# Kernel tuning notes

Hardware: AMD Instinct MI355X
Metric: run time of the kernel (lower is better)

## Reference

```python
import jax, jax.numpy as jnp
import numpy as np

EPS = 1e-5

def _ln(x, g, b):
    m = jnp.mean(x, axis=-1, keepdims=True)
    v = jnp.mean((x - m) ** 2, axis=-1, keepdims=True)
    return (x - m) * jax.lax.rsqrt(v + EPS) * g + b

def setup_inputs() -> dict:
    key = jax.random.key(0)
    B, T, V, D = 32, 512, 16, 128
    ks = jax.random.split(key, 22)
    rn = lambda k, shp, sc: jax.random.normal(k, shp, jnp.float32) * sc
    inp = {
        "x": rn(ks[0], (B, T, V), 1.0),
        # per-variable GRN params (stacked over the V variables)
        "W1": rn(ks[1], (V, D), 1.0),          # fc1: Linear(1, D) weight per var
        "b1": rn(ks[2], (V, D), 0.02),
        "W2": rn(ks[3], (V, D, D), 1.0 / np.sqrt(D)),   # fc2: Linear(D, D)
        "b2": rn(ks[4], (V, D), 0.02),
        "Wg": rn(ks[5], (V, D, D), 1.0 / np.sqrt(D)),   # gate: Linear(D, D)
        "bg": rn(ks[6], (V, D), 0.02),
        "Ws": rn(ks[7], (V, D), 1.0),          # skip: Linear(1, D)
        "bs": rn(ks[8], (V, D), 0.02),
        "gamma": jnp.ones((V, D), jnp.float32),
        "beta": jnp.zeros((V, D), jnp.float32),
        # softmax GRN params: d_in = V*D, d_hidden = D, d_out = V
        "sW1": rn(ks[9], (D, V * D), 1.0 / np.sqrt(V * D)),
        "sb1": rn(ks[10], (D,), 0.02),
        "sW2": rn(ks[11], (V, D), 1.0 / np.sqrt(D)),
        "sb2": rn(ks[12], (V,), 0.02),
        "sWg": rn(ks[13], (V, D), 1.0 / np.sqrt(D)),
        "sbg": rn(ks[14], (V,), 0.02),
        "sWs": rn(ks[15], (V, V * D), 1.0 / np.sqrt(V * D)),
        "sbs": rn(ks[16], (V,), 0.02),
        "sgamma": jnp.ones((V,), jnp.float32),
        "sbeta": jnp.zeros((V,), jnp.float32),
    }
    return inp

def reference(x, W1, b1, W2, b2, Wg, bg, Ws, bs, gamma, beta,
              sW1, sb1, sW2, sb2, sWg, sbg, sWs, sbs, sgamma, sbeta):
    V, D = W1.shape
    lead = x.shape[:-1]
    xf = x.reshape(-1, V)                                  # (N, V)
    # ---- all per-variable GRNs batched over the var dim ----
    h = jax.nn.elu(xf[..., None] * W1 + b1)                # (N, V, D)
    h2 = jnp.einsum('nvd,vod->nvo', h, W2) + b2            # (N, V, D)
    g = jax.nn.sigmoid(jnp.einsum('nvd,vod->nvo', h, Wg) + bg)
    skip = xf[..., None] * Ws + bs                         # (N, V, D)
    stacked = _ln(g * h2 + (1.0 - g) * skip, gamma, beta)  # (N, V, D)
    # ---- softmax GRN over flattened embeddings ----
    flat = stacked.reshape(-1, V * D)                      # (N, V*D)
    hs = jax.nn.elu(flat @ sW1.T + sb1)                    # (N, D)
    h2s = hs @ sW2.T + sb2                                 # (N, V)
    gs = jax.nn.sigmoid(hs @ sWg.T + sbg)
    sks = flat @ sWs.T + sbs
    weights = jax.nn.softmax(_ln(gs * h2s + (1.0 - gs) * sks, sgamma, sbeta), axis=-1)
    processed = jnp.einsum('nvd,nv->nd', stacked, weights) # (N, D)
    return processed.reshape(*lead, D), weights.reshape(*lead, V)
```

## Files before the change

### kernel.cpp

```cpp
#include <hip/hip_runtime.h>
#include <hip/hip_bf16.h>
#include <math.h>

#define NVAR 16
#define ND 128
#define NVD 2048
#define NROWS 16384
#define RTA 256
#define NRB 32

typedef short s16x8 __attribute__((ext_vector_type(8)));
typedef short s16x4 __attribute__((ext_vector_type(4)));
typedef float f32x4 __attribute__((ext_vector_type(4)));
typedef unsigned short u16;

#define MFMA(a,b,c) __builtin_amdgcn_mfma_f32_16x16x32_bf16((a),(b),(c),0,0,0)

#define OFF_W2  0
#define OFF_WG  262144
#define OFF_SW1 524288
#define OFF_SWS 786432
#define OFF_SW2 819200
#define OFF_SWG 821248
#define WS_ELEMS 823296
#define OFF_STK 823296
#define STK_ELEMS ((size_t)NROWS*NVD)
#define WS_NEEDED_BYTES (((size_t)WS_ELEMS + STK_ELEMS)*2)
#define SV_ELEMS ((size_t)(NROWS/16)*2048)

__device__ __forceinline__ unsigned f2bf(float f){
    union { float f; unsigned u; } c; c.f = f;
    unsigned u = c.u;
    u += 0x7fffu + ((u >> 16) & 1u);
    return u >> 16;
}
__device__ __forceinline__ float bf2f(unsigned bits){
    union { unsigned u; float f; } c; c.u = bits << 16;
    return c.f;
}
__device__ __forceinline__ float eluf(float x){ return x > 0.f ? x : __expf(x) - 1.f; }
__device__ __forceinline__ float sigm(float x){
    return __builtin_amdgcn_rcpf(1.f + __expf(-x));
}

__device__ __forceinline__ int offHs(int r, int c){
    return r*128 + ((((c>>3) ^ (r&7))<<3) | (c&7));
}
__device__ __forceinline__ int offBig(int r, int c){
    return r*2048 + ((((c>>3) ^ (r&7))<<3) | (c&7));
}

__global__ void prep_kernel(const float* __restrict__ W2, const float* __restrict__ Wg,
                            const float* __restrict__ sW1, const float* __restrict__ sWs,
                            const float* __restrict__ sW2, const float* __restrict__ sWg,
                            u16* __restrict__ ws){
    int i = blockIdx.x*256 + threadIdx.x;
    if (i >= WS_ELEMS) return;
    float v;
    if      (i < OFF_WG)  v = W2[i];
    else if (i < OFF_SW1) v = Wg[i-OFF_WG];
    else if (i < OFF_SWS) v = sW1[i-OFF_SW1];
    else if (i < OFF_SW2) v = sWs[i-OFF_SWS];
    else if (i < OFF_SWG) v = sW2[i-OFF_SW2];
    else                  v = sWg[i-OFF_SWG];
    ws[i] = (u16)f2bf(v);
}

__global__ __launch_bounds__(512, 2)
void vsn_varA(const float* __restrict__ x,
              const float* __restrict__ W1, const float* __restrict__ b1,
              const float* __restrict__ b2, const float* __restrict__ bg,
              const float* __restrict__ Wsk, const float* __restrict__ bsk,
              const float* __restrict__ gamma, const float* __restrict__ beta,
              u16* __restrict__ ws)
{
    __shared__ u16 lw2[128*128];
    __shared__ u16 lwg[128*128];
    __shared__ float lp[8*128];
    __shared__ float lxv[RTA];

    const int t = threadIdx.x, w = t>>6, l = t&63;
    const int hr = l>>4, c16 = l&15;
    const int v = blockIdx.y;
    const int row0 = blockIdx.x*RTA;

    #pragma unroll
    for (int i=0;i<8;++i){
        int cid = i*512 + t;
        int mat = cid>>11, within = cid&2047;
        int r = within>>4, c8 = within&15;
        const u16* src = ws + (mat? OFF_WG:OFF_W2) + v*16384 + r*128 + c8*8;
        s16x8 val = *reinterpret_cast<const s16x8*>(src);
        u16* dst = (mat? lwg:lw2) + r*128 + ((c8 ^ (r&7))<<3);
        *reinterpret_cast<s16x8*>(dst) = val;
    }
    if (t < 128){
        lp[t]     = W1[v*ND+t];    lp[128+t] = b1[v*ND+t];
        lp[256+t] = b2[v*ND+t];    lp[384+t] = bg[v*ND+t];
        lp[512+t] = Wsk[v*ND+t];   lp[640+t] = bsk[v*ND+t];
        lp[768+t] = gamma[v*ND+t]; lp[896+t] = beta[v*ND+t];
    }
    if (t < RTA) lxv[t] = x[(size_t)(row0+t)*NVAR + v];
    __syncthreads();

    #pragma unroll 1
    for (int pass=0; pass<2; ++pass){
        const int lrow0 = (w + pass*8)*16;
        const float xv = lxv[lrow0 + c16];

        s16x8 B[4];
        #pragma unroll
        for (int ks=0;ks<4;++ks){
            s16x8 o;
            #pragma unroll
            for (int j=0;j<8;++j){
                int c = ks*32 + hr*8 + j;
                o[j] = (short)f2bf(eluf(xv*lp[c] + lp[128+c]));
            }
            B[ks] = o;
        }
        __builtin_amdgcn_sched_barrier(0);

        float y[8][4];
        #pragma unroll
        for (int ct=0; ct<8; ++ct){
            f32x4 a2 = {0.f,0.f,0.f,0.f}, ag = {0.f,0.f,0.f,0.f};
            const int wr = ct*16 + c16;
            #pragma unroll
            for (int ks=0;ks<4;++ks){
                int chunk = (ks*4 + hr) ^ (wr&7);
                s16x8 A2 = *reinterpret_cast<const s16x8*>(lw2 + wr*128 + chunk*8);
                a2 = MFMA(A2, B[ks], a2);
            }
            #pragma unroll
            for (int ks=0;ks<4;++ks){
                int chunk = (ks*4 + hr) ^ (wr&7);
                s16x8 Ag = *reinterpret_cast<const s16x8*>(lwg + wr*128 + chunk*8);
                ag = MFMA(Ag, B[ks], ag);
            }
            const int obb = ct*16 + hr*4;
            float4 b2v = *reinterpret_cast<const float4*>(&lp[256+obb]);
            float4 bgv = *reinterpret_cast<const float4*>(&lp[384+obb]);
            float4 wsv = *reinterpret_cast<const float4*>(&lp[512+obb]);
            float4 bsv = *reinterpret_cast<const float4*>(&lp[640+obb]);
            #pragma unroll
            for (int j=0;j<4;++j){
                float h2 = a2[j] + reinterpret_cast<const float*>(&b2v)[j];
                float gg = sigm(ag[j] + reinterpret_cast<const float*>(&bgv)[j]);
                float sk = xv*reinterpret_cast<const float*>(&wsv)[j]
                           + reinterpret_cast<const float*>(&bsv)[j];
                y[ct][j] = gg*h2 + (1.f-gg)*sk;
            }
            __builtin_amdgcn_sched_barrier(0);
        }
        float s = 0.f, q = 0.f;
        #pragma unroll
        for (int ct=0;ct<8;++ct)
            #pragma unroll
            for (int j=0;j<4;++j){ float yy = y[ct][j]; s += yy; q += yy*yy; }
        s += __shfl_xor(s, 16); s += __shfl_xor(s, 32);
        q += __shfl_xor(q, 16); q += __shfl_xor(q, 32);
        float mean = s*(1.f/ND);
        float inv  = rsqrtf(q*(1.f/ND) - mean*mean + 1e-5f);

        const int grp = blockIdx.x*16 + w + pass*8;
        u16* stkb = ws + OFF_STK + (size_t)v*SV_ELEMS + (size_t)grp*2048;
        #pragma unroll
        for (int ctp=0; ctp<4; ++ctp){
            s16x4 o0, o1;
            {
                int ct = ctp*2;
                const int obb = ct*16 + hr*4;
                float4 gm = *reinterpret_cast<const float4*>(&lp[768+obb]);
                float4 bt = *reinterpret_cast<const float4*>(&lp[896+obb]);
                #pragma unroll
                for (int j=0;j<4;++j){
                    float z = (y[ct][j]-mean)*inv*reinterpret_cast<const float*>(&gm)[j]
                              + reinterpret_cast<const float*>(&bt)[j];
                    o0[j] = (short)f2bf(z);
                }
            }
            {
                int ct = ctp*2 + 1;
                const int obb = ct*16 + hr*4;
                float4 gm = *reinterpret_cast<const float4*>(&lp[768+obb]);
                float4 bt = *reinterpret_cast<const float4*>(&lp[896+obb]);
                #pragma unroll
                for (int j=0;j<4;++j){
                    float z = (y[ct][j]-mean)*inv*reinterpret_cast<const float*>(&gm)[j]
                              + reinterpret_cast<const float*>(&bt)[j];
                    o1[j] = (short)f2bf(z);
                }
            }
            u16* bp = stkb + ctp*512 + c16*32;
            *reinterpret_cast<s16x4*>(bp + hr*4)      = o0;
            *reinterpret_cast<s16x4*>(bp + 16 + hr*4) = o1;
            __builtin_amdgcn_sched_barrier(0);
        }
    }
}

__device__ __forceinline__ s16x8 ldA(const u16* abuf, int vrel, int rg, int ctp, int n, int hr){
    int base = (((vrel*2 + rg)*4 + ctp)*16 + n)*32;
    int fn = (n>>1)&3;
    return *reinterpret_cast<const s16x8*>(abuf + base + ((hr ^ fn)<<3));
}

__global__ __launch_bounds__(512, 4)
void vsn_softB(const u16* __restrict__ ws,
               const float* __restrict__ sb1, const float* __restrict__ sb2,
               const float* __restrict__ sbg, const float* __restrict__ sbs,
               const float* __restrict__ sgamma, const float* __restrict__ sbeta,
               float* __restrict__ out_proc, float* __restrict__ out_w)
{
    __shared__ u16   abuf[8192];
    __shared__ u16   hsb[32*128];
    __shared__ float pps_[4*32*16];
    __shared__ float pph[32*16];
    __shared__ float ppg[32*16];
    __shared__ float sksf[32*16];
    __shared__ float wgtb[32*16];

    float* pps = pps_;

    const int t = threadIdx.x, w = t>>6, l = t&63;
    const int hr = l>>4, c16 = l&15;
    const int row0 = blockIdx.x * NRB;
    const int grp0 = row0 >> 4;
    const int orow = w*16 + c16;
    const int rgs = w & 1;
    const int khf = w >> 1;

    const u16* stk  = ws + OFF_STK;
    const u16* sW1b = ws + OFF_SW1;
    const u16* sWsb = ws + OFF_SWS;

    f32x4 accHs[2] = {{0,0,0,0},{0,0,0,0}};
    f32x4 accSk = {0,0,0,0};

    #pragma unroll 1
    for (int kt=0; kt<8; ++kt){
        #pragma unroll
        for (int i=0;i<2;++i){
            int cid = i*512 + t;
            int vv  = kt*2 + (cid>>9);
            int rg  = (cid>>8)&1;
            int n   = (cid>>2)&15;
            int u   = cid&3;
            const u16* src = stk + (size_t)vv*SV_ELEMS + (size_t)(grp0+rg)*2048
                           + ((cid>>2)&63)*32 + u*8;
            s16x8 val = *reinterpret_cast<const s16x8*>(src);
            *reinterpret_cast<s16x8*>(abuf + (cid>>2)*32 + ((u ^ ((n>>1)&3))<<3)) = val;
        }
        __syncthreads();
        #pragma unroll
        for (int ks=0; ks<8; ++ks){
            s16x8 bf = *reinterpret_cast<const s16x8*>(
                sW1b + (size_t)orow*NVD + kt*256 + ks*32 + hr*8);
            #pragma unroll
            for (int rg=0; rg<2; ++rg){
                s16x8 af = ldA(abuf, ks>>2, rg, ks&3, c16, hr);
                accHs[rg] = MFMA(af, bf, accHs[rg]);
            }
        }
        #pragma unroll
        for (int kk=0; kk<2; ++kk){
            int ks = khf*2 + kk;
            s16x8 bf = *reinterpret_cast<const s16x8*>(
                sWsb + (size_t)c16*NVD + kt*256 + ks*32 + hr*8);
            s16x8 af = ldA(abuf, ks>>2, rgs, ks&3, c16, hr);
            accSk = MFMA(af, bf, accSk);
        }
        __syncthreads();
    }

    {
        float bb = sb1[orow];
        #pragma unroll
        for (int rg=0; rg<2; ++rg){
            #pragma unroll
            for (int j=0;j<4;++j){
                int r = rg*16 + hr*4 + j;
                hsb[offHs(r, orow)] = (u16)f2bf(eluf(accHs[rg][j] + bb));
            }
        }
        #pragma unroll
        for (int j=0;j<4;++j)
            pps[khf*512 + (rgs*16 + hr*4 + j)*16 + c16] = accSk[j];
    }
    __syncthreads();

    sksf[t] = pps[t] + pps[512+t] + pps[1024+t] + pps[1536+t] + sbs[t&15];
    if (w < 4){
        const u16* Bsrc = (w < 2) ? (ws + OFF_SW2) : (ws + OFF_SWG);
        int rg = w & 1;
        f32x4 acc = {0,0,0,0};
        #pragma unroll
        for (int ks=0; ks<4; ++ks){
            int rr = rg*16 + c16;
            int chunk = (ks*4 + hr) ^ (rr&7);
            s16x8 af = *reinterpret_cast<const s16x8*>(hsb + rr*128 + chunk*8);
            s16x8 bf = *reinterpret_cast<const s16x8*>(Bsrc + c16*ND + ks*32 + hr*8);
            acc = MFMA(af, bf, acc);
        }
        float* dst = (w < 2) ? pph : ppg;
        #pragma unroll
        for (int j=0;j<4;++j)
            dst[(rg*16 + hr*4 + j)*16 + c16] = acc[j];
    }
    __syncthreads();

    {
        int r = t>>4, vv = t & 15;
        float h2s = pph[r*16+vv] + sb2[vv];
        float gs  = sigm(ppg[r*16+vv] + sbg[vv]);
        float yv  = gs*h2s + (1.f-gs)*sksf[r*16+vv];
        float ssum = yv, qsum = yv*yv;
        #pragma unroll
        for (int m=1;m<16;m<<=1){ ssum += __shfl_xor(ssum,m,16); qsum += __shfl_xor(qsum,m,16); }
        float mean = ssum*(1.f/NVAR);
        float var  = qsum*(1.f/NVAR) - mean*mean;
        float z = (yv-mean)*rsqrtf(var+1e-5f)*sgamma[vv] + sbeta[vv];
        float mx = z;
        #pragma unroll
        for (int m=1;m<16;m<<=1) mx = fmaxf(mx, __shfl_xor(mx,m,16));
        float e = __expf(z-mx);
        float es = e;
        #pragma unroll
        for (int m=1;m<16;m<<=1) es += __shfl_xor(es,m,16);
        float wgt = e * __builtin_amdgcn_rcpf(es);
        wgtb[r*16+vv] = wgt;
        out_w[(size_t)(row0+r)*NVAR + vv] = wgt;
    }
    __syncthreads();

    {
        int r = t>>4, cu = t&15;
        int ctp = cu>>2, u = cu&3;
        int grp = (row0+r)>>4, n = r&15;
        float acc[8] = {0,0,0,0,0,0,0,0};
        #pragma unroll
        for (int v=0; v<NVAR; ++v){
            float wv = wgtb[r*16 + v];
            const u16* sp = stk + (size_t)v*SV_ELEMS + (size_t)grp*2048
                          + (ctp*16+n)*32 + u*8;
            s16x8 sv = *reinterpret_cast<const s16x8*>(sp);
            #pragma unroll
            for (int k=0;k<8;++k) acc[k] += bf2f((u16)sv[k]) * wv;
        }
        float* op = out_proc + (size_t)(row0+r)*ND + ctp*32 + u*8;
        float4 lo = { acc[0], acc[1], acc[2], acc[3] };
        float4 hi = { acc[4], acc[5], acc[6], acc[7] };
        *reinterpret_cast<float4*>(op)     = lo;
        *reinterpret_cast<float4*>(op + 4) = hi;
    }
}

__global__ __launch_bounds__(512, 4)
void vsn_fused(const float* __restrict__ x,
               const float* __restrict__ W1, const float* __restrict__ b1,
               const float* __restrict__ b2, const float* __restrict__ bg,
               const float* __restrict__ Wsk, const float* __restrict__ bsk,
               const float* __restrict__ gamma, const float* __restrict__ beta,
               const float* __restrict__ sb1, const float* __restrict__ sb2,
               const float* __restrict__ sbg, const float* __restrict__ sbs,
               const float* __restrict__ sgamma, const float* __restrict__ sbeta,
               const u16* __restrict__ ws,
               float* __restrict__ out_proc, float* __restrict__ out_w)
{
    __shared__ u16   big[16*2048];
    __shared__ u16   hsb[16*128];
    __shared__ float pp[8*256];
    __shared__ float psumbuf[256];
    __shared__ float sksbuf[256];
    __shared__ float sx[256];

    float* psum  = psumbuf;
    float* psum2 = psumbuf + 128;

    const int t   = threadIdx.x;
    const int w   = t >> 6;
    const int l   = t & 63;
    const int hr  = l >> 4;
    const int c16 = l & 15;
    const int row0 = blockIdx.x * 16;
    const int orow = w*16 + c16;

    if (t < 256) sx[t] = x[row0*NVAR + t];
    __syncthreads();

    const u16* W2b = ws + OFF_W2;
    const u16* Wgb = ws + OFF_WG;

    for (int v = 0; v < NVAR; ++v){
        #pragma unroll
        for (int i = 0; i < 4; ++i){
            int idx = i*512 + t;
            int r = idx >> 7, d = idx & 127;
            float hv = eluf(sx[r*NVAR+v]*W1[v*ND+d] + b1[v*ND+d]);
            big[offBig(r, v*ND+d)] = (u16)f2bf(hv);
        }
        __syncthreads();

        s16x8 A[4];
        #pragma unroll
        for (int ks = 0; ks < 4; ++ks)
            A[ks] = *reinterpret_cast<const s16x8*>(&big[offBig(c16, v*ND + ks*32 + hr*8)]);
        const s16x8* B2p = reinterpret_cast<const s16x8*>(W2b + v*ND*ND + orow*ND + hr*8);
        const s16x8* Bgp = reinterpret_cast<const s16x8*>(Wgb + v*ND*ND + orow*ND + hr*8);
        f32x4 acc2 = {0.f,0.f,0.f,0.f}, accg = {0.f,0.f,0.f,0.f};
        #pragma unroll
        for (int ks = 0; ks < 4; ++ks) acc2 = MFMA(A[ks], B2p[ks*4], acc2);
        #pragma unroll
        for (int ks = 0; ks < 4; ++ks) accg = MFMA(A[ks], Bgp[ks*4], accg);

        const float b2v = b2[v*ND+orow], bgv = bg[v*ND+orow];
        const float wsv = Wsk[v*ND+orow], bsv = bsk[v*ND+orow];
        float y[4];
        #pragma unroll
        for (int j = 0; j < 4; ++j){
            int r = hr*4 + j;
            float h2 = acc2[j] + b2v;
            float g  = sigm(accg[j] + bgv);
            float sk = sx[r*NVAR+v]*wsv + bsv;
            y[j] = g*h2 + (1.f-g)*sk;
        }
        float s[4], q[4];
        #pragma unroll
        for (int j=0;j<4;++j){ s[j]=y[j]; q[j]=y[j]*y[j]; }
        #pragma unroll
        for (int m=1; m<16; m<<=1){
            #pragma unroll
            for (int j=0;j<4;++j){
                s[j] += __shfl_xor(s[j], m, 16);
                q[j] += __shfl_xor(q[j], m, 16);
            }
        }
        if (c16 == 0){
            #pragma unroll
            for (int j=0;j<4;++j){
                psum [(hr*4+j)*8 + w] = s[j];
                psum2[(hr*4+j)*8 + w] = q[j];
            }
        }
        __syncthreads();

        if (t < 16){
            float ss=0.f, qq=0.f;
            #pragma unroll
            for (int ww=0; ww<8; ++ww){ ss += psum[t*8+ww]; qq += psum2[t*8+ww]; }
            float mean = ss*(1.f/ND);
            float var  = qq*(1.f/ND) - mean*mean;
            sksbuf[t]      = mean;
            sksbuf[16 + t] = rsqrtf(var + 1e-5f);
        }
        __syncthreads();

        const float gm = gamma[v*ND+orow], bt = beta[v*ND+orow];
        #pragma unroll
        for (int j=0;j<4;++j){
            int r = hr*4 + j;
            float z = (y[j]-sksbuf[r])*sksbuf[16+r]*gm + bt;
            big[offBig(r, v*ND+orow)] = (u16)f2bf(z);
        }
    }
    __syncthreads();

    const u16* sW1b = ws + OFF_SW1;
    {
        f32x4 acc0 = {0,0,0,0}, acc1 = {0,0,0,0};
        const s16x8* Bp = reinterpret_cast<const s16x8*>(sW1b + orow*NVD + hr*8);
        #pragma unroll 8
        for (int ks = 0; ks < 64; ks += 2){
            s16x8 A0 = *reinterpret_cast<const s16x8*>(&big[offBig(c16, ks*32 + hr*8)]);
            s16x8 A1 = *reinterpret_cast<const s16x8*>(&big[offBig(c16, (ks+1)*32 + hr*8)]);
            acc0 = MFMA(A0, Bp[ks*4],     acc0);
            acc1 = MFMA(A1, Bp[(ks+1)*4], acc1);
        }
        float bb = sb1[orow];
        #pragma unroll
        for (int j=0;j<4;++j){
            int r = hr*4 + j;
            hsb[offHs(r, orow)] = (u16)f2bf(eluf(acc0[j] + acc1[j] + bb));
        }
    }
    const u16* sWsb = ws + OFF_SWS;
    {
        f32x4 acc = {0,0,0,0};
        const s16x8* Bp = reinterpret_cast<const s16x8*>(sWsb + c16*NVD + hr*8);
        #pragma unroll
        for (int kk = 0; kk < 8; ++kk){
            int ks = w*8 + kk;
            s16x8 Af = *reinterpret_cast<const s16x8*>(&big[offBig(c16, ks*32 + hr*8)]);
            acc = MFMA(Af, Bp[ks*4], acc);
        }
        #pragma unroll
        for (int j=0;j<4;++j)
            pp[w*256 + (hr*4+j)*16 + c16] = acc[j];
    }
    __syncthreads();

    if (t < 256){
        float a = sbs[t & 15];
        #pragma unroll
        for (int ww=0; ww<8; ++ww) a += pp[ww*256 + t];
        sksbuf[t] = a;
    }
    __syncthreads();

    {
        const u16* Bsrc = (w < 4) ? (ws + OFF_SW2) : (ws + OFF_SWG);
        const int m = w & 3;
        s16x8 Af = *reinterpret_cast<const s16x8*>(&hsb[offHs(c16, m*32 + hr*8)]);
        s16x8 Bf = *reinterpret_cast<const s16x8*>(Bsrc + c16*ND + m*32 + hr*8);
        f32x4 z4 = {0,0,0,0};
        f32x4 acc = MFMA(Af, Bf, z4);
        #pragma unroll
        for (int j=0;j<4;++j)
            pp[w*256 + (hr*4+j)*16 + c16] = acc[j];
    }
    __syncthreads();

    if (t < 256){
        int r = t >> 4, vv = t & 15;
        float h2s = sb2[vv], gp = sbg[vv];
        #pragma unroll
        for (int j=0;j<4;++j){ h2s += pp[j*256 + t]; gp += pp[(4+j)*256 + t]; }
        float gs = sigm(gp);
        float yv = gs*h2s + (1.f-gs)*sksbuf[t];
        float ssum = yv, qsum = yv*yv;
        #pragma unroll
        for (int m=1;m<16;m<<=1){ ssum += __shfl_xor(ssum,m,16); qsum += __shfl_xor(qsum,m,16); }
        float mean = ssum*(1.f/NVAR);
        float var  = qsum*(1.f/NVAR) - mean*mean;
        float z = (yv-mean)*rsqrtf(var+1e-5f)*sgamma[vv] + sbeta[vv];
        float mx = z;
        #pragma unroll
        for (int m=1;m<16;m<<=1) mx = fmaxf(mx, __shfl_xor(mx,m,16));
        float e = __expf(z-mx);
        float es = e;
        #pragma unroll
        for (int m=1;m<16;m<<=1) es += __shfl_xor(es,m,16);
        float wgt = e/es;
        psumbuf[t] = wgt;
        out_w[(row0+r)*NVAR + vv] = wgt;
    }
    __syncthreads();

    if (t < 256){
        int r = t >> 4, d8 = (t & 15)*8;
        float acc[8] = {0,0,0,0,0,0,0,0};
        #pragma unroll
        for (int v=0; v<NVAR; ++v){
            float wv = psumbuf[r*NVAR + v];
            s16x8 sv = *reinterpret_cast<const s16x8*>(&big[offBig(r, v*ND + d8)]);
            #pragma unroll
            for (int k=0;k<8;++k) acc[k] += bf2f((u16)sv[k]) * wv;
        }
        float* op = &out_proc[(row0+r)*ND + d8];
        #pragma unroll
        for (int k=0;k<8;++k) op[k] = acc[k];
    }
}

extern "C" void kernel_launch(void* const* d_in, const int* in_sizes, int n_in,
                              void* d_out, int out_size, void* d_ws, size_t ws_size,
                              hipStream_t stream) {
    (void)in_sizes; (void)n_in; (void)out_size;
    const float* x     = (const float*)d_in[0];
    const float* W1    = (const float*)d_in[1];
    const float* b1    = (const float*)d_in[2];
    const float* W2    = (const float*)d_in[3];
    const float* b2    = (const float*)d_in[4];
    const float* Wg    = (const float*)d_in[5];
    const float* bg    = (const float*)d_in[6];
    const float* Wsk   = (const float*)d_in[7];
    const float* bsk   = (const float*)d_in[8];
    const float* gamma = (const float*)d_in[9];
    const float* beta  = (const float*)d_in[10];
    const float* sW1   = (const float*)d_in[11];
    const float* sb1   = (const float*)d_in[12];
    const float* sW2   = (const float*)d_in[13];
    const float* sb2   = (const float*)d_in[14];
    const float* sWg   = (const float*)d_in[15];
    const float* sbg   = (const float*)d_in[16];
    const float* sWs   = (const float*)d_in[17];
    const float* sbs   = (const float*)d_in[18];
    const float* sgam  = (const float*)d_in[19];
    const float* sbet  = (const float*)d_in[20];

    u16* ws = (u16*)d_ws;
    float* out_proc = (float*)d_out;
    float* out_w    = out_proc + (size_t)NROWS * ND;

    prep_kernel<<<(WS_ELEMS + 255)/256, 256, 0, stream>>>(W2, Wg, sW1, sWs, sW2, sWg, ws);

    if (ws_size >= WS_NEEDED_BYTES) {
        vsn_varA<<<dim3(NROWS/RTA, NVAR), 512, 0, stream>>>(
            x, W1, b1, b2, bg, Wsk, bsk, gamma, beta, ws);
        vsn_softB<<<NROWS/NRB, 512, 0, stream>>>(
            ws, sb1, sb2, sbg, sbs, sgam, sbet, out_proc, out_w);
    } else {
        vsn_fused<<<NROWS/16, 512, 0, stream>>>(
            x, W1, b1, b2, bg, Wsk, bsk, gamma, beta,
            sb1, sb2, sbg, sbs, sgam, sbet, ws, out_proc, out_w);
    }
}
```

Baseline: 114.8 us.

## Halve softB block size and give each wave a 32x32 output tile

```diff
diff --git a/kernel.cpp b/kernel.cpp
--- a/kernel.cpp
+++ b/kernel.cpp
@@ -206,7 +206,7 @@
     return *reinterpret_cast<const s16x8*>(abuf + base + ((hr ^ fn)<<3));
 }
 
-__global__ __launch_bounds__(512, 4)
+__global__ __launch_bounds__(256, 4)
 void vsn_softB(const u16* __restrict__ ws,
                const float* __restrict__ sb1, const float* __restrict__ sb2,
                const float* __restrict__ sbg, const float* __restrict__ sbs,
@@ -215,7 +215,7 @@
 {
     __shared__ u16   abuf[8192];
     __shared__ u16   hsb[32*128];
-    __shared__ float pps_[4*32*16];
+    __shared__ float pps_[2*32*16];
     __shared__ float pph[32*16];
     __shared__ float ppg[32*16];
     __shared__ float sksf[32*16];
@@ -227,7 +227,7 @@
     const int hr = l>>4, c16 = l&15;
     const int row0 = blockIdx.x * NRB;
     const int grp0 = row0 >> 4;
-    const int orow = w*16 + c16;
+    const int col0 = w*32;
     const int rgs = w & 1;
     const int khf = w >> 1;
 
@@ -235,19 +235,19 @@
     const u16* sW1b = ws + OFF_SW1;
     const u16* sWsb = ws + OFF_SWS;
 
-    f32x4 accHs[2] = {{0,0,0,0},{0,0,0,0}};
+    f32x4 accHs00 = {0,0,0,0}, accHs01 = {0,0,0,0};
+    f32x4 accHs10 = {0,0,0,0}, accHs11 = {0,0,0,0};
     f32x4 accSk = {0,0,0,0};
 
     #pragma unroll 1
     for (int kt=0; kt<8; ++kt){
         #pragma unroll
-        for (int i=0;i<2;++i){
-            int cid = i*512 + t;
+        for (int i=0;i<4;++i){
+            int cid = i*256 + t;
             int vv  = kt*2 + (cid>>9);
-            int rg  = (cid>>8)&1;
             int n   = (cid>>2)&15;
             int u   = cid&3;
-            const u16* src = stk + (size_t)vv*SV_ELEMS + (size_t)(grp0+rg)*2048
+            const u16* src = stk + (size_t)vv*SV_ELEMS + (size_t)(grp0+((cid>>8)&1))*2048
                            + ((cid>>2)&63)*32 + u*8;
             s16x8 val = *reinterpret_cast<const s16x8*>(src);
             *reinterpret_cast<s16x8*>(abuf + (cid>>2)*32 + ((u ^ ((n>>1)&3))<<3)) = val;
@@ -255,17 +255,19 @@
         __syncthreads();
         #pragma unroll
         for (int ks=0; ks<8; ++ks){
-            s16x8 bf = *reinterpret_cast<const s16x8*>(
-                sW1b + (size_t)orow*NVD + kt*256 + ks*32 + hr*8);
-            #pragma unroll
-            for (int rg=0; rg<2; ++rg){
-                s16x8 af = ldA(abuf, ks>>2, rg, ks&3, c16, hr);
-                accHs[rg] = MFMA(af, bf, accHs[rg]);
-            }
-        }
-        #pragma unroll
-        for (int kk=0; kk<2; ++kk){
-            int ks = khf*2 + kk;
+            const u16* bbase = sW1b + (size_t)(col0 + c16)*NVD + kt*256 + ks*32 + hr*8;
+            s16x8 bf0 = *reinterpret_cast<const s16x8*>(bbase);
+            s16x8 bf1 = *reinterpret_cast<const s16x8*>(bbase + (size_t)16*NVD);
+            s16x8 af0 = ldA(abuf, ks>>2, 0, ks&3, c16, hr);
+            s16x8 af1 = ldA(abuf, ks>>2, 1, ks&3, c16, hr);
+            accHs00 = MFMA(af0, bf0, accHs00);
+            accHs10 = MFMA(af1, bf0, accHs10);
+            accHs01 = MFMA(af0, bf1, accHs01);
+            accHs11 = MFMA(af1, bf1, accHs11);
+        }
+        #pragma unroll
+        for (int kk=0; kk<4; ++kk){
+            int ks = khf*4 + kk;
             s16x8 bf = *reinterpret_cast<const s16x8*>(
                 sWsb + (size_t)c16*NVD + kt*256 + ks*32 + hr*8);
             s16x8 af = ldA(abuf, ks>>2, rgs, ks&3, c16, hr);
@@ -275,14 +277,15 @@
     }
 
     {
-        float bb = sb1[orow];
-        #pragma unroll
-        for (int rg=0; rg<2; ++rg){
-            #pragma unroll
-            for (int j=0;j<4;++j){
-                int r = rg*16 + hr*4 + j;
-                hsb[offHs(r, orow)] = (u16)f2bf(eluf(accHs[rg][j] + bb));
-            }
+        float bb0 = sb1[col0 + c16];
+        float bb1 = sb1[col0 + 16 + c16];
+        #pragma unroll
+        for (int j=0;j<4;++j){
+            int r0 = hr*4 + j, r1 = 16 + hr*4 + j;
+            hsb[offHs(r0, col0 + c16)]      = (u16)f2bf(eluf(accHs00[j] + bb0));
+            hsb[offHs(r1, col0 + c16)]      = (u16)f2bf(eluf(accHs10[j] + bb0));
+            hsb[offHs(r0, col0 + 16 + c16)] = (u16)f2bf(eluf(accHs01[j] + bb1));
+            hsb[offHs(r1, col0 + 16 + c16)] = (u16)f2bf(eluf(accHs11[j] + bb1));
         }
         #pragma unroll
         for (int j=0;j<4;++j)
@@ -290,8 +293,12 @@
     }
     __syncthreads();
 
-    sksf[t] = pps[t] + pps[512+t] + pps[1024+t] + pps[1536+t] + sbs[t&15];
-    if (w < 4){
+    #pragma unroll
+    for (int i=0;i<2;++i){
+        int idx = i*256 + t;
+        sksf[idx] = pps[idx] + pps[512+idx] + sbs[idx&15];
+    }
+    {
         const u16* Bsrc = (w < 2) ? (ws + OFF_SW2) : (ws + OFF_SWG);
         int rg = w & 1;
         f32x4 acc = {0,0,0,0};
@@ -310,8 +317,9 @@
     }
     __syncthreads();
 
-    {
-        int r = t>>4, vv = t & 15;
+    #pragma unroll
+    for (int it=0; it<2; ++it){
+        int r = it*16 + (t>>4), vv = t & 15;
         float h2s = pph[r*16+vv] + sb2[vv];
         float gs  = sigm(ppg[r*16+vv] + sbg[vv]);
         float yv  = gs*h2s + (1.f-gs)*sksf[r*16+vv];
@@ -334,8 +342,10 @@
     }
     __syncthreads();
 
-    {
-        int r = t>>4, cu = t&15;
+    #pragma unroll
+    for (int it=0; it<2; ++it){
+        int idx = it*256 + t;
+        int r = idx>>4, cu = idx&15;
         int ctp = cu>>2, u = cu&3;
         int grp = (row0+r)>>4, n = r&15;
         float acc[8] = {0,0,0,0,0,0,0,0};
@@ -598,7 +608,7 @@
     if (ws_size >= WS_NEEDED_BYTES) {
         vsn_varA<<<dim3(NROWS/RTA, NVAR), 512, 0, stream>>>(
             x, W1, b1, b2, bg, Wsk, bsk, gamma, beta, ws);
-        vsn_softB<<<NROWS/NRB, 512, 0, stream>>>(
+        vsn_softB<<<NROWS/NRB, 256, 0, stream>>>(
             ws, sb1, sb2, sbg, sbs, sgam, sbet, out_proc, out_w);
     } else {
         vsn_fused<<<NROWS/16, 512, 0, stream>>>(
```

Measured after the change: 113.1 us. No clear change (-1.5%).

## Stage full stacked tile in LDS once and reuse it for final weighted sum

Applied to the files above, without the earlier changes.

```diff
diff --git a/kernel.cpp b/kernel.cpp
--- a/kernel.cpp
+++ b/kernel.cpp
@@ -200,20 +200,20 @@
     }
 }
 
-__device__ __forceinline__ s16x8 ldA(const u16* abuf, int vrel, int rg, int ctp, int n, int hr){
-    int base = (((vrel*2 + rg)*4 + ctp)*16 + n)*32;
+__device__ __forceinline__ s16x8 ldA(const u16* abuf, int v, int rg, int ctp, int n, int hr){
+    int base = (((v*2 + rg)*4 + ctp)*16 + n)*32;
     int fn = (n>>1)&3;
     return *reinterpret_cast<const s16x8*>(abuf + base + ((hr ^ fn)<<3));
 }
 
-__global__ __launch_bounds__(512, 4)
+__global__ __launch_bounds__(512, 1)
 void vsn_softB(const u16* __restrict__ ws,
                const float* __restrict__ sb1, const float* __restrict__ sb2,
                const float* __restrict__ sbg, const float* __restrict__ sbs,
                const float* __restrict__ sgamma, const float* __restrict__ sbeta,
                float* __restrict__ out_proc, float* __restrict__ out_w)
 {
-    __shared__ u16   abuf[8192];
+    __shared__ u16   abuf[65536];
     __shared__ u16   hsb[32*128];
     __shared__ float pps_[4*32*16];
     __shared__ float pph[32*16];
@@ -229,64 +229,61 @@
     const int grp0 = row0 >> 4;
     const int orow = w*16 + c16;
     const int rgs = w & 1;
-    const int khf = w >> 1;
+    const int kqs = w >> 1;
 
     const u16* stk  = ws + OFF_STK;
     const u16* sW1b = ws + OFF_SW1;
     const u16* sWsb = ws + OFF_SWS;
 
-    f32x4 accHs[2] = {{0,0,0,0},{0,0,0,0}};
+    #pragma unroll
+    for (int i=0;i<16;++i){
+        int cid = i*512 + t;
+        int vv  = cid>>9;
+        int n   = (cid>>2)&15;
+        int u   = cid&3;
+        const u16* src = stk + (size_t)vv*SV_ELEMS
+                       + (size_t)(grp0+((cid>>8)&1))*2048
+                       + (size_t)((cid>>2)&63)*32 + u*8;
+        s16x8 val = *reinterpret_cast<const s16x8*>(src);
+        *reinterpret_cast<s16x8*>(abuf + (cid>>2)*32 + ((u ^ ((n>>1)&3))<<3)) = val;
+    }
+    __syncthreads();
+
+    f32x4 accHs0 = {0,0,0,0}, accHs1 = {0,0,0,0};
+    {
+        const u16* bb = sW1b + (size_t)orow*NVD + hr*8;
+        #pragma unroll 8
+        for (int ks=0; ks<64; ++ks){
+            s16x8 bf = *reinterpret_cast<const s16x8*>(bb + ks*32);
+            s16x8 af0 = ldA(abuf, ks>>2, 0, ks&3, c16, hr);
+            s16x8 af1 = ldA(abuf, ks>>2, 1, ks&3, c16, hr);
+            accHs0 = MFMA(af0, bf, accHs0);
+            accHs1 = MFMA(af1, bf, accHs1);
+        }
+    }
     f32x4 accSk = {0,0,0,0};
-
-    #pragma unroll 1
-    for (int kt=0; kt<8; ++kt){
-        #pragma unroll
-        for (int i=0;i<2;++i){
-            int cid = i*512 + t;
-            int vv  = kt*2 + (cid>>9);
-            int rg  = (cid>>8)&1;
-            int n   = (cid>>2)&15;
-            int u   = cid&3;
-            const u16* src = stk + (size_t)vv*SV_ELEMS + (size_t)(grp0+rg)*2048
-                           + ((cid>>2)&63)*32 + u*8;
-            s16x8 val = *reinterpret_cast<const s16x8*>(src);
-            *reinterpret_cast<s16x8*>(abuf + (cid>>2)*32 + ((u ^ ((n>>1)&3))<<3)) = val;
-        }
-        __syncthreads();
-        #pragma unroll
-        for (int ks=0; ks<8; ++ks){
-            s16x8 bf = *reinterpret_cast<const s16x8*>(
-                sW1b + (size_t)orow*NVD + kt*256 + ks*32 + hr*8);
-            #pragma unroll
-            for (int rg=0; rg<2; ++rg){
-                s16x8 af = ldA(abuf, ks>>2, rg, ks&3, c16, hr);
-                accHs[rg] = MFMA(af, bf, accHs[rg]);
-            }
-        }
-        #pragma unroll
-        for (int kk=0; kk<2; ++kk){
-            int ks = khf*2 + kk;
-            s16x8 bf = *reinterpret_cast<const s16x8*>(
-                sWsb + (size_t)c16*NVD + kt*256 + ks*32 + hr*8);
+    {
+        const u16* bb = sWsb + (size_t)c16*NVD + hr*8;
+        #pragma unroll 8
+        for (int kk=0; kk<16; ++kk){
+            int ks = kqs*16 + kk;
+            s16x8 bf = *reinterpret_cast<const s16x8*>(bb + ks*32);
             s16x8 af = ldA(abuf, ks>>2, rgs, ks&3, c16, hr);
             accSk = MFMA(af, bf, accSk);
         }
-        __syncthreads();
     }
 
     {
         float bb = sb1[orow];
         #pragma unroll
-        for (int rg=0; rg<2; ++rg){
-            #pragma unroll
-            for (int j=0;j<4;++j){
-                int r = rg*16 + hr*4 + j;
-                hsb[offHs(r, orow)] = (u16)f2bf(eluf(accHs[rg][j] + bb));
-            }
+        for (int j=0;j<4;++j){
+            int r0 = hr*4 + j, r1 = 16 + hr*4 + j;
+            hsb[offHs(r0, orow)] = (u16)f2bf(eluf(accHs0[j] + bb));
+            hsb[offHs(r1, orow)] = (u16)f2bf(eluf(accHs1[j] + bb));
         }
         #pragma unroll
         for (int j=0;j<4;++j)
-            pps[khf*512 + (rgs*16 + hr*4 + j)*16 + c16] = accSk[j];
+            pps[kqs*512 + (rgs*16 + hr*4 + j)*16 + c16] = accSk[j];
     }
     __syncthreads();
 
@@ -337,13 +334,13 @@
     {
         int r = t>>4, cu = t&15;
         int ctp = cu>>2, u = cu&3;
-        int grp = (row0+r)>>4, n = r&15;
+        int rg = r>>4, n = r&15;
+        int fn = (n>>1)&3;
         float acc[8] = {0,0,0,0,0,0,0,0};
         #pragma unroll
         for (int v=0; v<NVAR; ++v){
             float wv = wgtb[r*16 + v];
-            const u16* sp = stk + (size_t)v*SV_ELEMS + (size_t)grp*2048
-                          + (ctp*16+n)*32 + u*8;
+            const u16* sp = abuf + (((v*2 + rg)*4 + ctp)*16 + n)*32 + ((u ^ fn)<<3);
             s16x8 sv = *reinterpret_cast<const s16x8*>(sp);
             #pragma unroll
             for (int k=0;k<8;++k) acc[k] += bf2f((u16)sv[k]) * wv;
```

Result: faster. 110.1 us (-4.1%).
